# Performance work log

Measured on AMD Instinct MI355X. Metric: run time of the kernel, lower is better.

Reference implementation:

```python
import jax, jax.numpy as jnp
import numpy as np

H = 16        # n_heads
D = 1024      # d_model
SPLIT = 4     # number of sequence blocks, each with its own MHA weights
DK = D // H   # head dim
B = 4
SEQ = 4096


def setup_inputs() -> dict:
    key = jax.random.key(0)
    ks = jax.random.split(key, 9)
    sc = 1.0 / np.sqrt(D).astype(np.float32)
    x = jax.random.normal(ks[0], (B, SEQ, D), jnp.float32)
    # Per-split projection weights (torch Linear applied as x @ W + b; random init so
    # the transpose convention is immaterial for a correctness baseline).
    Wq = jax.random.normal(ks[1], (SPLIT, D, D), jnp.float32) * sc
    Wk = jax.random.normal(ks[2], (SPLIT, D, D), jnp.float32) * sc
    Wv = jax.random.normal(ks[3], (SPLIT, D, D), jnp.float32) * sc
    Wo = jax.random.normal(ks[4], (SPLIT, D, D), jnp.float32) * sc
    bq = jax.random.normal(ks[5], (SPLIT, D), jnp.float32) * 0.02
    bk = jax.random.normal(ks[6], (SPLIT, D), jnp.float32) * 0.02
    bv = jax.random.normal(ks[7], (SPLIT, D), jnp.float32) * 0.02
    bo = jax.random.normal(ks[8], (SPLIT, D), jnp.float32) * 0.02
    return {"x": x, "Wq": Wq, "Wk": Wk, "Wv": Wv, "Wo": Wo,
            "bq": bq, "bk": bk, "bv": bv, "bo": bo}


def reference(x, Wq, Wk, Wv, Wo, bq, bk, bv, bo):
    b, l, d = x.shape
    L = l // SPLIT                     # block length
    xs = x.reshape(b, SPLIT, L, d)     # [b, s, L, d] block-diagonal structure

    def proj(W, bias):
        return jnp.einsum('bsld,sde->bsle', xs, W) + bias[None, :, None, :]

    q = proj(Wq, bq).reshape(b, SPLIT, L, H, DK)
    k = proj(Wk, bk).reshape(b, SPLIT, L, H, DK)
    v = proj(Wv, bv).reshape(b, SPLIT, L, H, DK)

    # scaled dot-product attention within each block, causal mask per block
    scores = jnp.einsum('bslhk,bsmhk->bshlm', q, k) / np.sqrt(DK).astype(np.float32)
    causal = jnp.tril(jnp.ones((L, L), dtype=bool))
    scores = jnp.where(causal[None, None, None], scores, jnp.float32(-1e9))
    attn = jax.nn.softmax(scores, axis=-1)   # dropout is identity in eval mode
    o = jnp.einsum('bshlm,bsmhk->bslhk', attn, v).reshape(b, SPLIT, L, d)

    out = jnp.einsum('bsld,sde->bsle', o, Wo) + bo[None, :, None, :]
    return out.reshape(b, l, d)
```

## Files before the change

### kernel.cpp

```cpp
#include <hip/hip_runtime.h>
#include <stdint.h>

#define H_ 16
#define D_ 1024
#define SPLIT_ 4
#define DK_ 64
#define B_ 4
#define SEQ_ 4096
#define L_ 1024

#define QSC 0.18033688f

typedef unsigned short ushort_t;
typedef __attribute__((ext_vector_type(8))) short short8;
typedef __attribute__((ext_vector_type(4))) float floatx4;
typedef __attribute__((ext_vector_type(4))) unsigned short ushortx4;

__device__ __forceinline__ ushort_t f2bf(float f) {
  union { float f; unsigned u; } cv; cv.f = f;
  unsigned u = cv.u;
  return (ushort_t)((u + 0x7fffu + ((u >> 16) & 1u)) >> 16);
}

__device__ __forceinline__ uint32_t pack_bf_trunc(float x, float y) {
#if __has_builtin(__builtin_amdgcn_perm)
  return __builtin_amdgcn_perm(__float_as_uint(y), __float_as_uint(x), 0x07060302u);
#else
  return (__float_as_uint(y) & 0xffff0000u) | (__float_as_uint(x) >> 16);
#endif
}

__device__ __forceinline__ float exp2f_fast(float x) {
#if __has_builtin(__builtin_amdgcn_exp2f)
  return __builtin_amdgcn_exp2f(x);
#else
  return exp2f(x);
#endif
}

__device__ __forceinline__ void gl2lds16(const ushort_t* g, ushort_t* l) {
  __builtin_amdgcn_global_load_lds(
      (const __attribute__((address_space(1))) uint32_t*)g,
      (__attribute__((address_space(3))) uint32_t*)l, 16, 0, 0);
}

__device__ __forceinline__ void wave_barrier() {
  asm volatile("" ::: "memory");
  __builtin_amdgcn_s_barrier();
  asm volatile("" ::: "memory");
}

__global__ __launch_bounds__(256) void convert_x(const float* __restrict__ X,
                                                 ushort_t* __restrict__ Y) {
  const int i = blockIdx.x * 256 + threadIdx.x;
  const float4 v = ((const float4*)X)[i];
  ushortx4 o;
  o[0] = f2bf(v.x); o[1] = f2bf(v.y); o[2] = f2bf(v.z); o[3] = f2bf(v.w);
  ((ushortx4*)Y)[i] = o;
}

__global__ __launch_bounds__(256) void wt_convert_all(const float* __restrict__ W0,
                                                      const float* __restrict__ W1,
                                                      const float* __restrict__ W2,
                                                      const float* __restrict__ W3,
                                                      ushort_t* __restrict__ Wt) {
  __shared__ ushort_t tile[32][33];
  const int z = blockIdx.z, mat = z >> 2, s = z & 3;
  const float* W = (mat == 0) ? W0 : (mat == 1) ? W1 : (mat == 2) ? W2 : W3;
  const float scale = (mat == 0) ? QSC : 1.0f;
  const float* Ws = W + (size_t)s * D_ * D_;
  ushort_t* Wts = Wt + ((size_t)mat * SPLIT_ + s) * D_ * D_;
  const int e0 = blockIdx.x * 32, d0 = blockIdx.y * 32;
  for (int i = threadIdx.y; i < 32; i += 8)
    tile[i][threadIdx.x] = f2bf(Ws[(size_t)(d0 + i) * D_ + e0 + threadIdx.x] * scale);
  __syncthreads();
  for (int i = threadIdx.y; i < 32; i += 8)
    Wts[(size_t)(e0 + i) * D_ + d0 + threadIdx.x] = tile[threadIdx.x][i];
}

__global__ __launch_bounds__(256) void gemm_qkv(const ushort_t* __restrict__ X,
                                                const ushort_t* __restrict__ Wt,
                                                const float* __restrict__ Bq,
                                                const float* __restrict__ Bk,
                                                const float* __restrict__ Bv,
                                                ushort_t* __restrict__ Qo,
                                                ushort_t* __restrict__ Ko,
                                                ushort_t* __restrict__ Vo) {
  __shared__ __attribute__((aligned(16))) ushort_t SH[20480];

  const size_t WT = (size_t)D_ * D_;
  const int xcd = blockIdx.x;
  const int u = blockIdx.y;
  const int bs = xcd + ((u >> 7) << 3);
  const int mn = u & 127;
  const int m0 = (mn >> 4) * 128;
  const int n0 = (mn & 15) * 64;
  const int s = bs & 3;
  const ushort_t* Xb = X + (size_t)bs * (L_ * D_);

  const int t = threadIdx.x;
  const int lane = t & 63;
  const int w = t >> 6;
  const int wm = w >> 1, wn = w & 1;
  const int quad = lane >> 4, cl = lane & 15;
  const int sw = (quad ^ (cl & 3)) * 8;

  floatx4 acc[3][4][2];
  floatx4 zero = {0.f, 0.f, 0.f, 0.f};
#pragma unroll
  for (int mt = 0; mt < 3; ++mt)
#pragma unroll
    for (int i = 0; i < 4; ++i)
#pragma unroll
      for (int j = 0; j < 2; ++j) acc[mt][i][j] = zero;

  const int c0 = t, c1 = t + 256;
  const int r0 = c0 >> 2, cc0 = ((c0 & 3) ^ (r0 & 3)) * 8;
  const int r1 = c1 >> 2, cc1 = ((c1 & 3) ^ (r1 & 3)) * 8;
  const ushort_t* A0 = Xb + (size_t)(m0 + r0) * D_ + cc0;
  const ushort_t* A1 = Xb + (size_t)(m0 + r1) * D_ + cc1;
  const ushort_t* Bsrc0 = Wt + (0 * SPLIT_ + s) * WT + (size_t)(n0 + r0) * D_ + cc0;
  const ushort_t* Bsrc1 = Wt + (1 * SPLIT_ + s) * WT + (size_t)(n0 + r0) * D_ + cc0;
  const ushort_t* Bsrc2 = Wt + (2 * SPLIT_ + s) * WT + (size_t)(n0 + r0) * D_ + cc0;

  auto STAGE = [&](int buf, int k0) {
    gl2lds16(A0 + k0, &SH[buf * 4096 + c0 * 8]);
    gl2lds16(A1 + k0, &SH[buf * 4096 + c1 * 8]);
    gl2lds16(Bsrc0 + k0, &SH[8192 + buf * 6144 + 0 * 2048 + t * 8]);
    gl2lds16(Bsrc1 + k0, &SH[8192 + buf * 6144 + 1 * 2048 + t * 8]);
    gl2lds16(Bsrc2 + k0, &SH[8192 + buf * 6144 + 2 * 2048 + t * 8]);
  };

  auto COMPUTE = [&](int buf) {
    const ushort_t* Ab = &SH[buf * 4096];
    const ushort_t* Bb = &SH[8192 + buf * 6144];
    short8 a[4];
#pragma unroll
    for (int i = 0; i < 4; ++i)
      a[i] = *(const short8*)&Ab[(wm * 64 + i * 16 + cl) * 32 + sw];
#pragma unroll
    for (int mt = 0; mt < 3; ++mt) {
      const ushort_t* Bm = Bb + mt * 2048;
      const short8 b0 = *(const short8*)&Bm[(wn * 32 + cl) * 32 + sw];
      const short8 b1 = *(const short8*)&Bm[(wn * 32 + 16 + cl) * 32 + sw];
#pragma unroll
      for (int i = 0; i < 4; ++i) {
        acc[mt][i][0] = __builtin_amdgcn_mfma_f32_16x16x32_bf16(a[i], b0, acc[mt][i][0], 0, 0, 0);
        acc[mt][i][1] = __builtin_amdgcn_mfma_f32_16x16x32_bf16(a[i], b1, acc[mt][i][1], 0, 0, 0);
      }
    }
  };

  STAGE(0, 0);
  for (int kt = 0; kt < 31; ++kt) {
    STAGE((kt + 1) & 1, (kt + 1) * 32);
    asm volatile("s_waitcnt vmcnt(5)" ::: "memory");
    wave_barrier();
    COMPUTE(kt & 1);
    wave_barrier();
  }
  asm volatile("s_waitcnt vmcnt(0)" ::: "memory");
  wave_barrier();
  COMPUTE(1);

  __syncthreads();
  ushort_t* CT = SH;

#pragma unroll
  for (int mt = 0; mt < 2; ++mt) {
    const float* bp = (mt == 0) ? Bq : Bk;
    ushort_t* Og = (mt == 0) ? Qo : Ko;
    const float bscale = (mt == 0) ? QSC : 1.0f;
    float bvj[2];
#pragma unroll
    for (int j = 0; j < 2; ++j)
      bvj[j] = bp[s * D_ + n0 + wn * 32 + j * 16 + cl] * bscale;
#pragma unroll
    for (int i = 0; i < 4; ++i)
#pragma unroll
      for (int j = 0; j < 2; ++j)
#pragma unroll
        for (int r = 0; r < 4; ++r) {
          const int row = wm * 64 + i * 16 + quad * 4 + r;
          const int col = wn * 32 + j * 16 + cl;
          const int ch = col >> 3, off = col & 7;
          CT[row * 64 + ((ch ^ (row & 7)) << 3) + off] = f2bf(acc[mt][i][j][r] + bvj[j]);
        }
    __syncthreads();
#pragma unroll
    for (int pass = 0; pass < 4; ++pass) {
      const int row = pass * 32 + (t >> 3);
      const int ck = t & 7;
      const short8 v = *(const short8*)&CT[row * 64 + ((ck ^ (row & 7)) << 3)];
      *(short8*)(Og + (size_t)bs * (L_ * D_) + (size_t)(m0 + row) * D_ + n0 + ck * 8) = v;
    }
    __syncthreads();
  }

  {
    float bvj[2];
#pragma unroll
    for (int j = 0; j < 2; ++j)
      bvj[j] = Bv[s * D_ + n0 + wn * 32 + j * 16 + cl];
#pragma unroll
    for (int i = 0; i < 4; ++i)
#pragma unroll
      for (int j = 0; j < 2; ++j)
#pragma unroll
        for (int r = 0; r < 4; ++r) {
          const int row = wn * 32 + j * 16 + cl;
          const int col = wm * 64 + i * 16 + quad * 4 + r;
          const int ch = col >> 3, off = col & 7;
          CT[row * 128 + ((ch ^ (row & 15)) << 3) + off] = f2bf(acc[2][i][j][r] + bvj[j]);
        }
    __syncthreads();
#pragma unroll
    for (int pass = 0; pass < 4; ++pass) {
      const int row = pass * 16 + (t >> 4);
      const int ck = t & 15;
      const short8 v = *(const short8*)&CT[row * 128 + ((ck ^ (row & 15)) << 3)];
      *(short8*)(Vo + (size_t)bs * (L_ * D_) + (size_t)(n0 + row) * L_ + m0 + ck * 8) = v;
    }
  }
}

template <int MODE>
__global__ __launch_bounds__(256) void gemm_bt(const ushort_t* __restrict__ X,
                                               const ushort_t* __restrict__ Wt,
                                               const float* __restrict__ bias,
                                               float bscale,
                                               void* __restrict__ Cv) {
  __shared__ __attribute__((aligned(16))) ushort_t SH[8192];
  ushort_t* As = SH;
  ushort_t* Bs = SH + 4096;

  const int xcd = blockIdx.x;
  const int u = blockIdx.y;
  const int bs = xcd + ((u >> 6) << 3);
  const int mn = u & 63;
  const int m0 = (mn >> 3) * 128;
  const int n0 = (mn & 7) * 128;
  const int s = bs & 3;
  const ushort_t* Xb = X + (size_t)bs * (L_ * D_);
  const ushort_t* Wts = Wt + (size_t)s * (D_ * D_);

  const int t = threadIdx.x;
  const int lane = t & 63;
  const int w = t >> 6;
  const int wm = w >> 1, wn = w & 1;
  const int quad = lane >> 4, cl = lane & 15;

  floatx4 acc[4][4];
  floatx4 zero = {0.f, 0.f, 0.f, 0.f};
#pragma unroll
  for (int i = 0; i < 4; ++i)
#pragma unroll
    for (int j = 0; j < 4; ++j) acc[i][j] = zero;

  const int c0 = t, c1 = t + 256;
  const int r0 = c0 >> 2, cc0 = ((c0 & 3) ^ (r0 & 3)) * 8;
  const int r1 = c1 >> 2, cc1 = ((c1 & 3) ^ (r1 & 3)) * 8;
  const int sw = (quad ^ (cl & 3)) * 8;

  for (int k0 = 0; k0 < D_; k0 += 32) {
    gl2lds16(Xb + (size_t)(m0 + r0) * D_ + k0 + cc0, &As[c0 * 8]);
    gl2lds16(Xb + (size_t)(m0 + r1) * D_ + k0 + cc1, &As[c1 * 8]);
    gl2lds16(Wts + (size_t)(n0 + r0) * D_ + k0 + cc0, &Bs[c0 * 8]);
    gl2lds16(Wts + (size_t)(n0 + r1) * D_ + k0 + cc1, &Bs[c1 * 8]);
    __syncthreads();
    short8 a[4], b[4];
#pragma unroll
    for (int i = 0; i < 4; ++i)
      a[i] = *(const short8*)&As[(wm * 64 + i * 16 + cl) * 32 + sw];
#pragma unroll
    for (int j = 0; j < 4; ++j)
      b[j] = *(const short8*)&Bs[(wn * 64 + j * 16 + cl) * 32 + sw];
#pragma unroll
    for (int i = 0; i < 4; ++i)
#pragma unroll
      for (int j = 0; j < 4; ++j)
        acc[i][j] = __builtin_amdgcn_mfma_f32_16x16x32_bf16(a[i], b[j], acc[i][j], 0, 0, 0);
    __syncthreads();
  }

  float bvj[4];
#pragma unroll
  for (int j = 0; j < 4; ++j)
    bvj[j] = bias[s * D_ + n0 + wn * 64 + j * 16 + cl] * bscale;

  if (MODE == 2) {
#pragma unroll
    for (int j = 0; j < 4; ++j) {
      const int col = n0 + wn * 64 + j * 16 + cl;
#pragma unroll
      for (int i = 0; i < 4; ++i) {
        const int rb = m0 + wm * 64 + i * 16 + quad * 4;
        float* Cf = (float*)Cv + (size_t)bs * (L_ * D_) + (size_t)rb * D_ + col;
#pragma unroll
        for (int r = 0; r < 4; ++r) Cf[(size_t)r * D_] = acc[i][j][r] + bvj[j];
      }
    }
    return;
  }

  ushort_t* CT = SH;
#pragma unroll
  for (int ph = 0; ph < 2; ++ph) {
    __syncthreads();
    if (MODE == 0 ? (wm == ph) : (wn == ph)) {
#pragma unroll
      for (int i = 0; i < 4; ++i)
#pragma unroll
        for (int j = 0; j < 4; ++j)
#pragma unroll
          for (int r = 0; r < 4; ++r) {
            int row, col;
            if (MODE == 0) { row = i * 16 + quad * 4 + r; col = wn * 64 + j * 16 + cl; }
            else           { row = j * 16 + cl;           col = wm * 64 + i * 16 + quad * 4 + r; }
            const int ch = col >> 3, off = col & 7;
            CT[row * 128 + ((ch ^ (row & 15)) << 3) + off] = f2bf(acc[i][j][r] + bvj[j]);
          }
    }
    __syncthreads();
#pragma unroll
    for (int pass = 0; pass < 4; ++pass) {
      const int row = pass * 16 + (t >> 4);
      const int ck = t & 15;
      const short8 v = *(const short8*)&CT[row * 128 + ((ck ^ (row & 15)) << 3)];
      if (MODE == 0) {
        *(short8*)((ushort_t*)Cv + (size_t)bs * (L_ * D_) +
                   (size_t)(m0 + ph * 64 + row) * D_ + n0 + ck * 8) = v;
      } else {
        *(short8*)((ushort_t*)Cv + (size_t)bs * (L_ * D_) +
                   (size_t)(n0 + ph * 64 + row) * L_ + m0 + ck * 8) = v;
      }
    }
  }
}

__device__ __forceinline__ void attn_step(const ushort_t* __restrict__ Kbuf,
                                          const ushort_t* __restrict__ Vbuf,
                                          ushort_t* __restrict__ PTw,
                                          const short8 qa0, const short8 qa1,
                                          floatx4 (&o)[4], float& m_i, float& l_i,
                                          const bool diag, const int w,
                                          const int quad, const int cl) {
  floatx4 zero = {0.f, 0.f, 0.f, 0.f};
  const int sw0 = (quad ^ (cl & 7)) * 8;
  const int sw1 = ((4 + quad) ^ (cl & 7)) * 8;

  floatx4 st[4];
#pragma unroll
  for (int j = 0; j < 4; ++j) {
    const int row = (j * 16 + cl) * 64;
    const short8 ka0 = *(const short8*)&Kbuf[row + sw0];
    const short8 ka1 = *(const short8*)&Kbuf[row + sw1];
    floatx4 z = zero;
    z = __builtin_amdgcn_mfma_f32_16x16x32_bf16(ka0, qa0, z, 0, 0, 0);
    z = __builtin_amdgcn_mfma_f32_16x16x32_bf16(ka1, qa1, z, 0, 0, 0);
    st[j] = z;
  }

  if (diag) {
    const int ql = w * 16 + cl;
#pragma unroll
    for (int j = 0; j < 4; ++j)
#pragma unroll
      for (int r = 0; r < 4; ++r)
        if (j * 16 + quad * 4 + r > ql) st[j][r] = -1e30f;
  }

  float tm = fmaxf(fmaxf(fmaxf(st[0][0], st[0][1]), fmaxf(st[0][2], st[0][3])),
                   fmaxf(fmaxf(st[1][0], st[1][1]), fmaxf(st[1][2], st[1][3])));
  tm = fmaxf(tm, fmaxf(fmaxf(fmaxf(st[2][0], st[2][1]), fmaxf(st[2][2], st[2][3])),
                       fmaxf(fmaxf(st[3][0], st[3][1]), fmaxf(st[3][2], st[3][3]))));
  tm = fmaxf(tm, __shfl_xor(tm, 16, 64));
  tm = fmaxf(tm, __shfl_xor(tm, 32, 64));
  const float mnew = fmaxf(m_i, tm);
  const float alpha = exp2f_fast(m_i - mnew);
  m_i = mnew;

  float tsv = 0.f;
#pragma unroll
  for (int j = 0; j < 4; ++j)
#pragma unroll
    for (int r = 0; r < 4; ++r) {
      st[j][r] = exp2f_fast(st[j][r] - mnew);
      tsv += st[j][r];
    }
  tsv += __shfl_xor(tsv, 16, 64);
  tsv += __shfl_xor(tsv, 32, 64);
  l_i = l_i * alpha + tsv;

#pragma unroll
  for (int j = 0; j < 4; ++j) {
    const int base = cl * 72 + j * 16 + quad * 4;
    *(uint32_t*)&PTw[base] = pack_bf_trunc(st[j][0], st[j][1]);
    *(uint32_t*)&PTw[base + 2] = pack_bf_trunc(st[j][2], st[j][3]);
  }

#pragma unroll
  for (int j = 0; j < 4; ++j)
#pragma unroll
    for (int r = 0; r < 4; ++r) o[j][r] *= alpha;

  const short8 pb0 = *(const short8*)&PTw[cl * 72 + quad * 8];
  const short8 pb1 = *(const short8*)&PTw[cl * 72 + 32 + quad * 8];
#pragma unroll
  for (int j = 0; j < 4; ++j) {
    const int row = (j * 16 + cl) * 64;
    const short8 va0 = *(const short8*)&Vbuf[row + sw0];
    const short8 va1 = *(const short8*)&Vbuf[row + sw1];
    o[j] = __builtin_amdgcn_mfma_f32_16x16x32_bf16(va0, pb0, o[j], 0, 0, 0);
    o[j] = __builtin_amdgcn_mfma_f32_16x16x32_bf16(va1, pb1, o[j], 0, 0, 0);
  }
}

__device__ __forceinline__ void attn_store(ushort_t* __restrict__ O, size_t act_base,
                                           int qt, int h, const floatx4 (&o)[4],
                                           float l_i, int w, int quad, int cl) {
  const float inv = 1.0f / l_i;
  ushort_t* Orow = O + act_base + (size_t)(qt * 64 + w * 16 + cl) * D_ + h * DK_;
#pragma unroll
  for (int j = 0; j < 4; ++j) {
    ushortx4 pk;
#pragma unroll
    for (int r = 0; r < 4; ++r) pk[r] = f2bf(o[j][r] * inv);
    *(ushortx4*)(Orow + j * 16 + quad * 4) = pk;
  }
}

__global__ __launch_bounds__(256) void attn_kernel(const ushort_t* __restrict__ Q,
                                                   const ushort_t* __restrict__ K,
                                                   const ushort_t* __restrict__ Vt,
                                                   ushort_t* __restrict__ O) {
  __shared__ __attribute__((aligned(16))) ushort_t Ks[2][64 * 64];
  __shared__ __attribute__((aligned(16))) ushort_t Vts[2][64 * 64];
  __shared__ __attribute__((aligned(16))) ushort_t PT[8][1152];

  const int p = blockIdx.x, h = blockIdx.y, bs = blockIdx.z;
  const int t = threadIdx.x, lane = t & 63, w = t >> 6;
  const int quad = lane >> 4, cl = lane & 15;
  const size_t act_base = (size_t)bs * (L_ * D_);
  const int qtA = p, qtB = 15 - p;
  const int NIT = 16 - p;

  const int cA = t, cB = t + 256;
  const int rA = cA >> 3, ccA = ((cA & 7) ^ (rA & 7)) * 8;
  const int rB = cB >> 3, ccB = ((cB & 7) ^ (rB & 7)) * 8;

  const ushort_t* pKA = K + act_base + (size_t)rA * D_ + h * DK_ + ccA;
  const ushort_t* pKB = K + act_base + (size_t)rB * D_ + h * DK_ + ccB;
  const ushort_t* pVA = Vt + act_base + (size_t)(h * DK_ + rA) * L_ + ccA;
  const ushort_t* pVB = Vt + act_base + (size_t)(h * DK_ + rB) * L_ + ccB;
  const size_t kstep = (size_t)64 * D_, vstep = 64;

  floatx4 zero = {0.f, 0.f, 0.f, 0.f};

  const ushort_t* QpA = Q + act_base + (size_t)(qtA * 64 + w * 16 + cl) * D_ + h * DK_ + quad * 8;
  const ushort_t* QpB = Q + act_base + (size_t)(qtB * 64 + w * 16 + cl) * D_ + h * DK_ + quad * 8;
  const short8 qaA0 = *(const short8*)QpA;
  const short8 qaA1 = *(const short8*)(QpA + 32);
  const short8 qaB0 = *(const short8*)QpB;
  const short8 qaB1 = *(const short8*)(QpB + 32);

  floatx4 oA[4], oB[4];
#pragma unroll
  for (int j = 0; j < 4; ++j) { oA[j] = zero; oB[j] = zero; }
  float mA = -3.0e38f, lA = 0.f, mB = -3.0e38f, lB = 0.f;

  gl2lds16(pKA, &Ks[0][cA * 8]);
  gl2lds16(pKB, &Ks[0][cB * 8]);
  gl2lds16(pVA, &Vts[0][cA * 8]);
  gl2lds16(pVB, &Vts[0][cB * 8]);

  for (int kv = 0; kv < NIT; ++kv) {
    __syncthreads();
    if (kv + 1 < NIT) {
      pKA += kstep; pKB += kstep; pVA += vstep; pVB += vstep;
      const int nb = (kv + 1) & 1;
      gl2lds16(pKA, &Ks[nb][cA * 8]);
      gl2lds16(pKB, &Ks[nb][cB * 8]);
      gl2lds16(pVA, &Vts[nb][cA * 8]);
      gl2lds16(pVB, &Vts[nb][cB * 8]);
    }
    const int buf = kv & 1;

    if (kv <= p) {
      attn_step(Ks[buf], Vts[buf], PT[w], qaA0, qaA1, oA, mA, lA,
                kv == p, w, quad, cl);
      if (kv == p) attn_store(O, act_base, qtA, h, oA, lA, w, quad, cl);
    }
    attn_step(Ks[buf], Vts[buf], PT[w + 4], qaB0, qaB1, oB, mB, lB,
              kv == NIT - 1, w, quad, cl);
  }
  attn_store(O, act_base, qtB, h, oB, lB, w, quad, cl);
}

extern "C" void kernel_launch(void* const* d_in, const int* in_sizes, int n_in,
                              void* d_out, int out_size, void* d_ws, size_t ws_size,
                              hipStream_t stream) {
  const float* x  = (const float*)d_in[0];
  const float* Wq = (const float*)d_in[1];
  const float* Wk = (const float*)d_in[2];
  const float* Wv = (const float*)d_in[3];
  const float* Wo = (const float*)d_in[4];
  const float* bq = (const float*)d_in[5];
  const float* bk = (const float*)d_in[6];
  const float* bv = (const float*)d_in[7];
  const float* bo = (const float*)d_in[8];

  const size_t WT_SZ = (size_t)SPLIT_ * D_ * D_;
  const size_t ACT_SZ = (size_t)B_ * SEQ_ * D_;

  ushort_t* ws0 = (ushort_t*)d_ws;
  ushort_t* xbf = ws0;
  ushort_t* wtall = xbf + ACT_SZ;
  ushort_t* wto = wtall + 3 * WT_SZ;
  ushort_t* Vtb = wtall + 4 * WT_SZ;
  ushort_t* Qb = (ushort_t*)d_out;
  ushort_t* Kb = Qb + ACT_SZ;
  ushort_t* Ob = xbf;

  convert_x<<<ACT_SZ / 1024, 256, 0, stream>>>(x, xbf);
  wt_convert_all<<<dim3(32, 32, 16), dim3(32, 8, 1), 0, stream>>>(Wq, Wk, Wv, Wo, wtall);

  gemm_qkv<<<dim3(8, 256, 1), dim3(256, 1, 1), 0, stream>>>(
      xbf, wtall, bq, bk, bv, Qb, Kb, Vtb);

  dim3 ag(8, 16, 16);
  attn_kernel<<<ag, dim3(256, 1, 1), 0, stream>>>(Qb, Kb, Vtb, Ob);

  gemm_bt<2><<<dim3(8, 128, 1), dim3(256, 1, 1), 0, stream>>>(Ob, wto, bo, 1.0f, d_out);
}
```

Baseline: 453.3 us.

## Triple-buffer QKV and output GEMM K-loops and reorder QKV tile mapping

Moves the QKV GEMM from a double-buffered to a triple-buffered global-to-LDS pipeline, keeping two stages in flight through a relaxed vmcnt wait. It replaces the output-projection GEMM, which synchronized twice per k-step with a single buffer, with a triple-buffered pipeline that uses wave-level barriers. The QKV tile index mapping is swapped so consecutive blocks share an N tile across M tiles, which should improve weight reuse in L2. The cost is more LDS per block, which may lower occupancy.

```diff
diff --git a/kernel.cpp b/kernel.cpp
--- a/kernel.cpp
+++ b/kernel.cpp
@@ -86,15 +86,15 @@
                                                 ushort_t* __restrict__ Qo,
                                                 ushort_t* __restrict__ Ko,
                                                 ushort_t* __restrict__ Vo) {
-  __shared__ __attribute__((aligned(16))) ushort_t SH[20480];
+  __shared__ __attribute__((aligned(16))) ushort_t SH[30720];
 
   const size_t WT = (size_t)D_ * D_;
   const int xcd = blockIdx.x;
   const int u = blockIdx.y;
   const int bs = xcd + ((u >> 7) << 3);
   const int mn = u & 127;
-  const int m0 = (mn >> 4) * 128;
-  const int n0 = (mn & 15) * 64;
+  const int m0 = (mn & 7) * 128;
+  const int n0 = (mn >> 3) * 64;
   const int s = bs & 3;
   const ushort_t* Xb = X + (size_t)bs * (L_ * D_);
 
@@ -126,14 +126,14 @@
   auto STAGE = [&](int buf, int k0) {
     gl2lds16(A0 + k0, &SH[buf * 4096 + c0 * 8]);
     gl2lds16(A1 + k0, &SH[buf * 4096 + c1 * 8]);
-    gl2lds16(Bsrc0 + k0, &SH[8192 + buf * 6144 + 0 * 2048 + t * 8]);
-    gl2lds16(Bsrc1 + k0, &SH[8192 + buf * 6144 + 1 * 2048 + t * 8]);
-    gl2lds16(Bsrc2 + k0, &SH[8192 + buf * 6144 + 2 * 2048 + t * 8]);
+    gl2lds16(Bsrc0 + k0, &SH[12288 + buf * 6144 + 0 * 2048 + t * 8]);
+    gl2lds16(Bsrc1 + k0, &SH[12288 + buf * 6144 + 1 * 2048 + t * 8]);
+    gl2lds16(Bsrc2 + k0, &SH[12288 + buf * 6144 + 2 * 2048 + t * 8]);
   };
 
   auto COMPUTE = [&](int buf) {
     const ushort_t* Ab = &SH[buf * 4096];
-    const ushort_t* Bb = &SH[8192 + buf * 6144];
+    const ushort_t* Bb = &SH[12288 + buf * 6144];
     short8 a[4];
 #pragma unroll
     for (int i = 0; i < 4; ++i)
@@ -152,13 +152,23 @@
   };
 
   STAGE(0, 0);
-  for (int kt = 0; kt < 31; ++kt) {
-    STAGE((kt + 1) & 1, (kt + 1) * 32);
-    asm volatile("s_waitcnt vmcnt(5)" ::: "memory");
-    wave_barrier();
-    COMPUTE(kt & 1);
-    wave_barrier();
-  }
+  STAGE(1, 32);
+#define QKV_STEP(SB, CB, KS)                              \
+  STAGE(SB, (KS)*32);                                     \
+  asm volatile("s_waitcnt vmcnt(10)" ::: "memory");       \
+  wave_barrier();                                         \
+  COMPUTE(CB);                                            \
+  wave_barrier();
+  for (int k3 = 0; k3 < 30; k3 += 3) {
+    QKV_STEP(2, 0, k3 + 2)
+    QKV_STEP(0, 1, k3 + 3)
+    QKV_STEP(1, 2, k3 + 4)
+  }
+#undef QKV_STEP
+  asm volatile("s_waitcnt vmcnt(5)" ::: "memory");
+  wave_barrier();
+  COMPUTE(0);
+  wave_barrier();
   asm volatile("s_waitcnt vmcnt(0)" ::: "memory");
   wave_barrier();
   COMPUTE(1);
@@ -224,15 +234,11 @@
   }
 }
 
-template <int MODE>
-__global__ __launch_bounds__(256) void gemm_bt(const ushort_t* __restrict__ X,
-                                               const ushort_t* __restrict__ Wt,
-                                               const float* __restrict__ bias,
-                                               float bscale,
-                                               void* __restrict__ Cv) {
-  __shared__ __attribute__((aligned(16))) ushort_t SH[8192];
-  ushort_t* As = SH;
-  ushort_t* Bs = SH + 4096;
+__global__ __launch_bounds__(256) void gemm_o(const ushort_t* __restrict__ X,
+                                              const ushort_t* __restrict__ Wt,
+                                              const float* __restrict__ bias,
+                                              float* __restrict__ C) {
+  __shared__ __attribute__((aligned(16))) ushort_t SH[24576];
 
   const int xcd = blockIdx.x;
   const int u = blockIdx.y;
@@ -249,6 +255,7 @@
   const int w = t >> 6;
   const int wm = w >> 1, wn = w & 1;
   const int quad = lane >> 4, cl = lane & 15;
+  const int sw = (quad ^ (cl & 3)) * 8;
 
   floatx4 acc[4][4];
   floatx4 zero = {0.f, 0.f, 0.f, 0.f};
@@ -260,14 +267,21 @@
   const int c0 = t, c1 = t + 256;
   const int r0 = c0 >> 2, cc0 = ((c0 & 3) ^ (r0 & 3)) * 8;
   const int r1 = c1 >> 2, cc1 = ((c1 & 3) ^ (r1 & 3)) * 8;
-  const int sw = (quad ^ (cl & 3)) * 8;
-
-  for (int k0 = 0; k0 < D_; k0 += 32) {
-    gl2lds16(Xb + (size_t)(m0 + r0) * D_ + k0 + cc0, &As[c0 * 8]);
-    gl2lds16(Xb + (size_t)(m0 + r1) * D_ + k0 + cc1, &As[c1 * 8]);
-    gl2lds16(Wts + (size_t)(n0 + r0) * D_ + k0 + cc0, &Bs[c0 * 8]);
-    gl2lds16(Wts + (size_t)(n0 + r1) * D_ + k0 + cc1, &Bs[c1 * 8]);
-    __syncthreads();
+  const ushort_t* A0 = Xb + (size_t)(m0 + r0) * D_ + cc0;
+  const ushort_t* A1 = Xb + (size_t)(m0 + r1) * D_ + cc1;
+  const ushort_t* B0 = Wts + (size_t)(n0 + r0) * D_ + cc0;
+  const ushort_t* B1 = Wts + (size_t)(n0 + r1) * D_ + cc1;
+
+  auto STAGE = [&](int buf, int k0) {
+    gl2lds16(A0 + k0, &SH[buf * 4096 + c0 * 8]);
+    gl2lds16(A1 + k0, &SH[buf * 4096 + c1 * 8]);
+    gl2lds16(B0 + k0, &SH[12288 + buf * 4096 + c0 * 8]);
+    gl2lds16(B1 + k0, &SH[12288 + buf * 4096 + c1 * 8]);
+  };
+
+  auto COMPUTE = [&](int buf) {
+    const ushort_t* As = &SH[buf * 4096];
+    const ushort_t* Bs = &SH[12288 + buf * 4096];
     short8 a[4], b[4];
 #pragma unroll
     for (int i = 0; i < 4; ++i)
@@ -280,60 +294,44 @@
 #pragma unroll
       for (int j = 0; j < 4; ++j)
         acc[i][j] = __builtin_amdgcn_mfma_f32_16x16x32_bf16(a[i], b[j], acc[i][j], 0, 0, 0);
-    __syncthreads();
-  }
+  };
+
+  STAGE(0, 0);
+  STAGE(1, 32);
+#define O_STEP(SB, CB, KS)                                \
+  STAGE(SB, (KS)*32);                                     \
+  asm volatile("s_waitcnt vmcnt(8)" ::: "memory");        \
+  wave_barrier();                                         \
+  COMPUTE(CB);                                            \
+  wave_barrier();
+  for (int k3 = 0; k3 < 30; k3 += 3) {
+    O_STEP(2, 0, k3 + 2)
+    O_STEP(0, 1, k3 + 3)
+    O_STEP(1, 2, k3 + 4)
+  }
+#undef O_STEP
+  asm volatile("s_waitcnt vmcnt(4)" ::: "memory");
+  wave_barrier();
+  COMPUTE(0);
+  wave_barrier();
+  asm volatile("s_waitcnt vmcnt(0)" ::: "memory");
+  wave_barrier();
+  COMPUTE(1);
 
   float bvj[4];
 #pragma unroll
   for (int j = 0; j < 4; ++j)
-    bvj[j] = bias[s * D_ + n0 + wn * 64 + j * 16 + cl] * bscale;
-
-  if (MODE == 2) {
-#pragma unroll
-    for (int j = 0; j < 4; ++j) {
-      const int col = n0 + wn * 64 + j * 16 + cl;
-#pragma unroll
-      for (int i = 0; i < 4; ++i) {
-        const int rb = m0 + wm * 64 + i * 16 + quad * 4;
-        float* Cf = (float*)Cv + (size_t)bs * (L_ * D_) + (size_t)rb * D_ + col;
-#pragma unroll
-        for (int r = 0; r < 4; ++r) Cf[(size_t)r * D_] = acc[i][j][r] + bvj[j];
-      }
-    }
-    return;
-  }
-
-  ushort_t* CT = SH;
-#pragma unroll
-  for (int ph = 0; ph < 2; ++ph) {
-    __syncthreads();
-    if (MODE == 0 ? (wm == ph) : (wn == ph)) {
-#pragma unroll
-      for (int i = 0; i < 4; ++i)
-#pragma unroll
-        for (int j = 0; j < 4; ++j)
-#pragma unroll
-          for (int r = 0; r < 4; ++r) {
-            int row, col;
-            if (MODE == 0) { row = i * 16 + quad * 4 + r; col = wn * 64 + j * 16 + cl; }
-            else           { row = j * 16 + cl;           col = wm * 64 + i * 16 + quad * 4 + r; }
-            const int ch = col >> 3, off = col & 7;
-            CT[row * 128 + ((ch ^ (row & 15)) << 3) + off] = f2bf(acc[i][j][r] + bvj[j]);
-          }
-    }
-    __syncthreads();
-#pragma unroll
-    for (int pass = 0; pass < 4; ++pass) {
-      const int row = pass * 16 + (t >> 4);
-      const int ck = t & 15;
-      const short8 v = *(const short8*)&CT[row * 128 + ((ck ^ (row & 15)) << 3)];
-      if (MODE == 0) {
-        *(short8*)((ushort_t*)Cv + (size_t)bs * (L_ * D_) +
-                   (size_t)(m0 + ph * 64 + row) * D_ + n0 + ck * 8) = v;
-      } else {
-        *(short8*)((ushort_t*)Cv + (size_t)bs * (L_ * D_) +
-                   (size_t)(n0 + ph * 64 + row) * L_ + m0 + ck * 8) = v;
-      }
+    bvj[j] = bias[s * D_ + n0 + wn * 64 + j * 16 + cl];
+
+#pragma unroll
+  for (int j = 0; j < 4; ++j) {
+    const int col = n0 + wn * 64 + j * 16 + cl;
+#pragma unroll
+    for (int i = 0; i < 4; ++i) {
+      const int rb = m0 + wm * 64 + i * 16 + quad * 4;
+      float* Cf = C + (size_t)bs * (L_ * D_) + (size_t)rb * D_ + col;
+#pragma unroll
+      for (int r = 0; r < 4; ++r) Cf[(size_t)r * D_] = acc[i][j][r] + bvj[j];
     }
   }
 }
@@ -531,5 +529,5 @@
   dim3 ag(8, 16, 16);
   attn_kernel<<<ag, dim3(256, 1, 1), 0, stream>>>(Qb, Kb, Vtb, Ob);
 
-  gemm_bt<2><<<dim3(8, 128, 1), dim3(256, 1, 1), 0, stream>>>(Ob, wto, bo, 1.0f, d_out);
-}
+  gemm_o<<<dim3(8, 128, 1), dim3(256, 1, 1), 0, stream>>>(Ob, wto, bo, (float*)d_out);
+}
```

Result: faster. 429.9 us (-5.2%).
